# Performance work log

Measured on AMD Instinct MI355X. Metric: run time of the kernel, lower is better.

The kernel has to match this reference:

```python
import jax, jax.numpy as jnp
import numpy as np

N_NODES = 1_000_000
N_UPD = 200_000
D_MEM = 172
D_MSG = 172


def setup_inputs() -> dict:
    key = jax.random.key(0)
    ks = jax.random.split(key, 8)
    memory = jax.random.normal(ks[0], (N_NODES, D_MEM), dtype=jnp.float32)
    last_update = jnp.zeros((N_NODES,), dtype=jnp.float32)
    # unique node ids (no duplicates, as guaranteed by the caller in the original code)
    unique_node_ids = jax.random.permutation(ks[1], N_NODES)[:N_UPD].astype(jnp.int64)
    unique_messages = jax.random.normal(ks[2], (N_UPD, D_MSG), dtype=jnp.float32)
    timestamps = jax.random.uniform(ks[3], (N_UPD,), dtype=jnp.float32) * 1e6
    s_ih = 1.0 / np.sqrt(D_MEM)
    weight_ih = jax.random.uniform(ks[4], (3 * D_MEM, D_MSG), jnp.float32, -s_ih, s_ih)
    weight_hh = jax.random.uniform(ks[5], (3 * D_MEM, D_MEM), jnp.float32, -s_ih, s_ih)
    bias_ih = jax.random.uniform(ks[6], (3 * D_MEM,), jnp.float32, -s_ih, s_ih)
    bias_hh = jax.random.uniform(ks[7], (3 * D_MEM,), jnp.float32, -s_ih, s_ih)
    return {
        "memory": memory,
        "last_update": last_update,
        "unique_node_ids": unique_node_ids,
        "unique_messages": unique_messages,
        "timestamps": timestamps,
        "weight_ih": weight_ih,
        "weight_hh": weight_hh,
        "bias_ih": bias_ih,
        "bias_hh": bias_hh,
    }


def _gru_cell(x, h, weight_ih, weight_hh, bias_ih, bias_hh):
    # PyTorch GRUCell, gate order: reset, update, new
    gi = x @ weight_ih.T + bias_ih          # [M, 3H]
    gh = h @ weight_hh.T + bias_hh          # [M, 3H]
    i_r, i_z, i_n = jnp.split(gi, 3, axis=-1)
    h_r, h_z, h_n = jnp.split(gh, 3, axis=-1)
    r = jax.nn.sigmoid(i_r + h_r)
    z = jax.nn.sigmoid(i_z + h_z)
    n = jnp.tanh(i_n + r * h_n)
    return n + z * (h - n)                  # (1-z)*n + z*h


def reference(memory, last_update, unique_node_ids, unique_messages, timestamps,
              weight_ih, weight_hh, bias_ih, bias_hh):
    # gather rows of the node memory for the updated nodes
    h = memory[unique_node_ids]                                   # [M, D]
    h_new = _gru_cell(unique_messages, h, weight_ih, weight_hh, bias_ih, bias_hh)
    # scatter updated rows back (ids are unique)
    updated_memory = memory.at[unique_node_ids].set(h_new)        # [N, D]
    updated_last_update = last_update.at[unique_node_ids].set(timestamps)
    # original module returns memory with the singleton middle dim restored
    return updated_memory[:, None, :], updated_last_update
```

## Files before the change

### kernel.cpp

```cpp
#include <hip/hip_runtime.h>

typedef __attribute__((ext_vector_type(8))) short short8;
typedef __attribute__((ext_vector_type(4))) float f32x4;

#define N_NODES 1000000
#define N_UPD   200000
#define D       172
#define BM      64
#define LDA     360
#define KSTEPS  11
#define NTILES  48
#define KSLICE  (NTILES*512)
#define GRU_BLOCKS (N_UPD / BM)
#define NM4 43000000
#define BPACK_USHORTS (KSTEPS*KSLICE)
#define BIAS_OFF  (BPACK_USHORTS*2)
#define MASK_OFF  (BIAS_OFF + 688*4)
#define WS_NEED   (MASK_OFF + N_NODES)

__device__ __forceinline__ unsigned short f2bf(float f) {
  union { float f; unsigned u; } v; v.f = f;
  unsigned r = v.u + 0x7FFFu + ((v.u >> 16) & 1u);
  return (unsigned short)(r >> 16);
}
__device__ __forceinline__ float bf2f(unsigned short h) {
  union { unsigned u; float f; } v; v.u = ((unsigned)h) << 16;
  return v.f;
}
__device__ __forceinline__ ushort4 f2bf4(float4 v) {
  return make_ushort4(f2bf(v.x), f2bf(v.y), f2bf(v.z), f2bf(v.w));
}

__device__ __forceinline__ void gld16(const unsigned short* g, unsigned short* l) {
  __builtin_amdgcn_global_load_lds(
      (const __attribute__((address_space(1))) unsigned int*)g,
      (__attribute__((address_space(3))) unsigned int*)l, 16, 0, 0);
}

__global__ void prep_kernel(const float* __restrict__ wih, const float* __restrict__ whh,
                            const float* __restrict__ bih, const float* __restrict__ bhh,
                            unsigned short* __restrict__ Bpack, float* __restrict__ bias4,
                            uint4* __restrict__ mask16) {
  int gid = blockIdx.x * 256 + threadIdx.x;
  if (gid < 688) {
    int which = gid / 172, j = gid % 172;
    float v;
    if (which == 0)      v = bih[j]       + bhh[j];
    else if (which == 1) v = bih[172 + j] + bhh[172 + j];
    else if (which == 2) v = bih[344 + j];
    else                 v = bhh[344 + j];
    bias4[gid] = v;
  }
  if (gid < N_NODES / 16) mask16[gid] = make_uint4(0, 0, 0, 0);
  if (gid >= BPACK_USHORTS) return;
  int e  = gid & 7;
  int l  = (gid >> 3) & 63;
  int nt = (gid >> 9) % NTILES;
  int ks = gid / KSLICE;
  int k  = ks * 32 + ((l >> 4) << 3) + e;
  int c  = l & 15;
  int w  = nt / 12, tl = nt % 12;
  int gate = tl / 3, ti = tl % 3;
  int j = w * 48 + ti * 16 + c;
  float v = 0.f;
  if (j < D) {
    if (gate == 0) {
      if (k < D)        v = wih[j * D + k];
      else if (k < 2*D) v = whh[j * D + (k - D)];
    } else if (gate == 1) {
      if (k < D)        v = wih[(D + j) * D + k];
      else if (k < 2*D) v = whh[(D + j) * D + (k - D)];
    } else if (gate == 2) {
      if (k < D)        v = wih[(2*D + j) * D + k];
    } else {
      if (k >= D && k < 2*D) v = whh[(2*D + j) * D + (k - D)];
    }
  }
  Bpack[gid] = f2bf(v);
}

__global__ void mask_set_kernel(const int* __restrict__ ids, unsigned char* __restrict__ mask) {
  int i = blockIdx.x * 256 + threadIdx.x;
  if (i < N_UPD) mask[ids[i]] = 1;
}

__global__ void copy_kernel(const float4* __restrict__ mem4, const float4* __restrict__ lu4,
                            float4* __restrict__ out4, float4* __restrict__ outlu4) {
  const long NL4 = N_NODES / 4;
  long stride = (long)gridDim.x * blockDim.x;
  for (long i = (long)blockIdx.x * blockDim.x + threadIdx.x; i < NM4 + NL4; i += stride) {
    if (i < NM4) out4[i] = mem4[i];
    else         outlu4[i - NM4] = lu4[i - NM4];
  }
}

__global__ __launch_bounds__(256)
void copy_masked_kernel(const float4* __restrict__ mem4, const float* __restrict__ lu,
                        const unsigned char* __restrict__ mask,
                        float4* __restrict__ out4, float* __restrict__ outlu) {
  const unsigned stride = gridDim.x * 256;
  for (unsigned i = blockIdx.x * 256 + threadIdx.x; i < NM4; i += stride) {
    unsigned row = i / 43u;
    if (!mask[row]) out4[i] = mem4[i];
  }
  for (unsigned j = blockIdx.x * 256 + threadIdx.x; j < N_NODES; j += stride) {
    if (!mask[j]) outlu[j] = lu[j];
  }
}

__global__ __launch_bounds__(512, 2)
void gru64_kernel(const float* __restrict__ memory, const float* __restrict__ msgs,
                  const int* __restrict__ ids, const float* __restrict__ ts,
                  const unsigned short* __restrict__ Bpack, const float* __restrict__ bias4,
                  float* __restrict__ out_mem, float* __restrict__ out_lu) {
  __shared__ unsigned short At[BM * LDA];
  __shared__ unsigned short Bl[2][KSLICE];
  const int tid  = threadIdx.x;
  const int m0   = blockIdx.x * BM;
  const int wave = tid >> 6, lane = tid & 63;
  const int g = lane >> 4, c = lane & 15;
  const int wm = wave >> 2, wc = wave & 3;

  {
    const unsigned short* src = Bpack;
    #pragma unroll
    for (int i = 0; i < 6; ++i) {
      int off = (wave * 6 + i) * 512 + lane * 8;
      gld16(src + off, &Bl[0][0] + off);
    }
  }

  const float4* x4 = (const float4*)msgs + (size_t)m0 * 43;
  float4 xv[6], hv[6];
  #pragma unroll
  for (int i = 0; i < 6; ++i) {
    int s = tid + i * 512;
    if (i < 5 || s < 2752) xv[i] = x4[s];
  }
  #pragma unroll
  for (int i = 0; i < 6; ++i) {
    int s = tid + i * 512;
    if (i < 5 || s < 2752) {
      int row = s / 43, seg = s - row * 43;
      int nid = ids[m0 + row];
      hv[i] = ((const float4*)(memory + (size_t)nid * D))[seg];
    }
  }
  #pragma unroll
  for (int i = 0; i < 6; ++i) {
    int s = tid + i * 512;
    if (i < 5 || s < 2752) {
      int row = s / 43, seg = s - row * 43;
      *(ushort4*)&At[row * LDA + seg * 4]       = f2bf4(xv[i]);
      *(ushort4*)&At[row * LDA + 172 + seg * 4] = f2bf4(hv[i]);
    }
  }
  if (tid < BM) {
    *(uint4*)&At[tid * LDA + 344] = make_uint4(0, 0, 0, 0);
    int nid = ids[m0 + tid];
    out_lu[nid] = ts[m0 + tid];
  }
  __syncthreads();

  f32x4 C0_0={0,0,0,0}, C0_1={0,0,0,0}, C0_2={0,0,0,0}, C0_3={0,0,0,0};
  f32x4 C0_4={0,0,0,0}, C0_5={0,0,0,0}, C0_6={0,0,0,0}, C0_7={0,0,0,0};
  f32x4 C0_8={0,0,0,0}, C0_9={0,0,0,0}, C0_10={0,0,0,0}, C0_11={0,0,0,0};
  f32x4 C1_0={0,0,0,0}, C1_1={0,0,0,0}, C1_2={0,0,0,0}, C1_3={0,0,0,0};
  f32x4 C1_4={0,0,0,0}, C1_5={0,0,0,0}, C1_6={0,0,0,0}, C1_7={0,0,0,0};
  f32x4 C1_8={0,0,0,0}, C1_9={0,0,0,0}, C1_10={0,0,0,0}, C1_11={0,0,0,0};

  const int ar0 = (wm * 32 + c) * LDA;
  const int ar1 = (wm * 32 + 16 + c) * LDA;

#define MMSTEP(NT) { short8 b = bb[(NT)*64]; \
    C0_##NT = __builtin_amdgcn_mfma_f32_16x16x32_bf16(a0, b, C0_##NT, 0, 0, 0); \
    C1_##NT = __builtin_amdgcn_mfma_f32_16x16x32_bf16(a1, b, C1_##NT, 0, 0, 0); }
  int cur = 0;
  #pragma unroll 1
  for (int ks = 0; ks < KSTEPS; ++ks) {
    if (ks + 1 < KSTEPS) {
      const unsigned short* src = Bpack + (size_t)(ks + 1) * KSLICE;
      unsigned short* dst = &Bl[cur ^ 1][0];
      #pragma unroll
      for (int i = 0; i < 6; ++i) {
        int off = (wave * 6 + i) * 512 + lane * 8;
        gld16(src + off, dst + off);
      }
    }
    short8 a0 = *(const short8*)&At[ar0 + ks * 32 + g * 8];
    short8 a1 = *(const short8*)&At[ar1 + ks * 32 + g * 8];
    const short8* bb = (const short8*)&Bl[cur][wc * 12 * 512 + lane * 8];
    MMSTEP(0)  MMSTEP(1)  MMSTEP(2)  MMSTEP(3)
    MMSTEP(4)  MMSTEP(5)  MMSTEP(6)  MMSTEP(7)
    MMSTEP(8)  MMSTEP(9)  MMSTEP(10) MMSTEP(11)
    __syncthreads();
    cur ^= 1;
  }
#undef MMSTEP

#define DO_TI(TI, CR, CZ, CI, CH) { int j = wc * 48 + (TI) * 16 + c; if (j < D) { \
      float rp = CR[r] + bias4[j];        float zp = CZ[r] + bias4[172 + j];      \
      float ip = CI[r] + bias4[344 + j];  float hp = CH[r] + bias4[516 + j];      \
      float ho = bf2f(hrow[j]);                                                   \
      float rr = 1.f / (1.f + __expf(-rp));                                       \
      float zz = 1.f / (1.f + __expf(-zp));                                       \
      float e2 = __expf(2.f * (ip + rr * hp));                                    \
      float nn = 1.f - 2.f / (e2 + 1.f);                                          \
      orow[j] = nn + zz * (ho - nn); } }
  #pragma unroll
  for (int r = 0; r < 4; ++r) {
    {
      const int row_local = wm * 32 + g * 4 + r;
      float* orow = out_mem + (size_t)ids[m0 + row_local] * D;
      const unsigned short* hrow = &At[row_local * LDA + 172];
      DO_TI(0, C0_0, C0_3, C0_6, C0_9)
      DO_TI(1, C0_1, C0_4, C0_7, C0_10)
      DO_TI(2, C0_2, C0_5, C0_8, C0_11)
    }
    {
      const int row_local = wm * 32 + 16 + g * 4 + r;
      float* orow = out_mem + (size_t)ids[m0 + row_local] * D;
      const unsigned short* hrow = &At[row_local * LDA + 172];
      DO_TI(0, C1_0, C1_3, C1_6, C1_9)
      DO_TI(1, C1_1, C1_4, C1_7, C1_10)
      DO_TI(2, C1_2, C1_5, C1_8, C1_11)
    }
  }
#undef DO_TI
}

extern "C" void kernel_launch(void* const* d_in, const int* in_sizes, int n_in,
                              void* d_out, int out_size, void* d_ws, size_t ws_size,
                              hipStream_t stream) {
  const float* memory      = (const float*)d_in[0];
  const float* last_update = (const float*)d_in[1];
  const int*   ids         = (const int*)  d_in[2];
  const float* msgs        = (const float*)d_in[3];
  const float* ts          = (const float*)d_in[4];
  const float* wih         = (const float*)d_in[5];
  const float* whh         = (const float*)d_in[6];
  const float* bih         = (const float*)d_in[7];
  const float* bhh         = (const float*)d_in[8];

  float* out_mem = (float*)d_out;
  float* out_lu  = out_mem + (size_t)N_NODES * D;

  unsigned short* Bpack = (unsigned short*)d_ws;
  float* bias4 = (float*)((char*)d_ws + BIAS_OFF);
  unsigned char* mask = (unsigned char*)d_ws + MASK_OFF;

  prep_kernel<<<BPACK_USHORTS / 256, 256, 0, stream>>>(wih, whh, bih, bhh, Bpack, bias4,
                                                       (uint4*)mask);
  if (ws_size >= WS_NEED) {
    mask_set_kernel<<<(N_UPD + 255) / 256, 256, 0, stream>>>(ids, mask);
    copy_masked_kernel<<<2048, 256, 0, stream>>>((const float4*)memory, last_update, mask,
                                                 (float4*)out_mem, out_lu);
  } else {
    copy_kernel<<<4096, 256, 0, stream>>>((const float4*)memory, (const float4*)last_update,
                                          (float4*)out_mem, (float4*)out_lu);
  }
  gru64_kernel<<<GRU_BLOCKS, 512, 0, stream>>>(memory, msgs, ids, ts, Bpack, bias4,
                                               out_mem, out_lu);
}
```

Before: 589.3 us.

## Fuse masked copy and GRU into one interleaved kernel with larger tiles

Merges the masked memory copy and the GRU kernel into a single launch whose blocks are interleaved between copy work and GRU tiles, so bandwidth-bound copying overlaps with MFMA compute. The GRU tile grows from 64 to 96 rows with 768 threads, and the B-slice double buffer in LDS is replaced by a single buffer that is prefetched through registers and guarded by two barriers per k-step. The aim is to cut the separate copy pass's serialization and raise occupancy, at the cost of extra barriers and tail guards.

```diff
diff --git a/kernel.cpp b/kernel.cpp
--- a/kernel.cpp
+++ b/kernel.cpp
@@ -6,12 +6,17 @@
 #define N_NODES 1000000
 #define N_UPD   200000
 #define D       172
-#define BM      64
+#define BM      96
+#define THREADS 768
 #define LDA     360
 #define KSTEPS  11
 #define NTILES  48
 #define KSLICE  (NTILES*512)
-#define GRU_BLOCKS (N_UPD / BM)
+#define NGRU    2084
+#define NGRU_G  261
+#define NCOPY_G 512
+#define NCOPY_BLOCKS 4096
+#define COPY_THREADS (NCOPY_BLOCKS*THREADS)
 #define NM4 43000000
 #define BPACK_USHORTS (KSTEPS*KSLICE)
 #define BIAS_OFF  (BPACK_USHORTS*2)
@@ -30,7 +35,6 @@
 __device__ __forceinline__ ushort4 f2bf4(float4 v) {
   return make_ushort4(f2bf(v.x), f2bf(v.y), f2bf(v.z), f2bf(v.w));
 }
-
 __device__ __forceinline__ void gld16(const unsigned short* g, unsigned short* l) {
   __builtin_amdgcn_global_load_lds(
       (const __attribute__((address_space(1))) unsigned int*)g,
@@ -94,71 +98,75 @@
   }
 }
 
-__global__ __launch_bounds__(256)
-void copy_masked_kernel(const float4* __restrict__ mem4, const float* __restrict__ lu,
-                        const unsigned char* __restrict__ mask,
-                        float4* __restrict__ out4, float* __restrict__ outlu) {
-  const unsigned stride = gridDim.x * 256;
-  for (unsigned i = blockIdx.x * 256 + threadIdx.x; i < NM4; i += stride) {
-    unsigned row = i / 43u;
-    if (!mask[row]) out4[i] = mem4[i];
-  }
-  for (unsigned j = blockIdx.x * 256 + threadIdx.x; j < N_NODES; j += stride) {
-    if (!mask[j]) outlu[j] = lu[j];
-  }
-}
-
-__global__ __launch_bounds__(512, 2)
-void gru64_kernel(const float* __restrict__ memory, const float* __restrict__ msgs,
-                  const int* __restrict__ ids, const float* __restrict__ ts,
-                  const unsigned short* __restrict__ Bpack, const float* __restrict__ bias4,
-                  float* __restrict__ out_mem, float* __restrict__ out_lu) {
+__global__ __launch_bounds__(THREADS, 3)
+void fused_kernel(const float* __restrict__ memory, const float* __restrict__ last_update,
+                  const float* __restrict__ msgs, const int* __restrict__ ids,
+                  const float* __restrict__ ts, const unsigned short* __restrict__ Bpack,
+                  const float* __restrict__ bias4, const unsigned char* __restrict__ mask,
+                  float* __restrict__ out_mem, float* __restrict__ out_lu, int ncopyg) {
   __shared__ unsigned short At[BM * LDA];
-  __shared__ unsigned short Bl[2][KSLICE];
-  const int tid  = threadIdx.x;
-  const int m0   = blockIdx.x * BM;
+  __shared__ unsigned short Bl[KSLICE];
+  const int tid = threadIdx.x;
+  const int g8 = blockIdx.x >> 3, b7 = blockIdx.x & 7;
+
+  int sub; bool is_copy = false;
+  if (ncopyg) {
+    int r = g8 % 3, q = g8 / 3;
+    if (r == 0) sub = q;
+    else { is_copy = true; sub = q * 2 + (r - 1); if (sub >= NCOPY_G) return; }
+  } else sub = g8;
+
+  if (is_copy) {
+    const int cblk = sub * 8 + b7;
+    const float4* mem4 = (const float4*)memory;
+    float4* out4 = (float4*)out_mem;
+    for (unsigned i = (unsigned)cblk * THREADS + tid; i < NM4; i += COPY_THREADS) {
+      unsigned row = i / 43u;
+      if (!mask[row]) out4[i] = mem4[i];
+    }
+    for (unsigned j = (unsigned)cblk * THREADS + tid; j < N_NODES; j += COPY_THREADS) {
+      if (!mask[j]) out_lu[j] = last_update[j];
+    }
+    return;
+  }
+
+  const int idx = sub * 8 + b7;
+  const int m0  = idx * BM;
+  if (m0 >= N_UPD) return;
   const int wave = tid >> 6, lane = tid & 63;
   const int g = lane >> 4, c = lane & 15;
   const int wm = wave >> 2, wc = wave & 3;
 
-  {
-    const unsigned short* src = Bpack;
-    #pragma unroll
-    for (int i = 0; i < 6; ++i) {
-      int off = (wave * 6 + i) * 512 + lane * 8;
-      gld16(src + off, &Bl[0][0] + off);
-    }
-  }
-
+  #pragma unroll
+  for (int i = 0; i < 4; ++i) {
+    int off = (wave * 4 + i) * 512 + lane * 8;
+    gld16(Bpack + off, &Bl[0] + off);
+  }
+
+  const int vlim = min(BM * 43, (N_UPD - m0) * 43);
   const float4* x4 = (const float4*)msgs + (size_t)m0 * 43;
   float4 xv[6], hv[6];
   #pragma unroll
   for (int i = 0; i < 6; ++i) {
-    int s = tid + i * 512;
-    if (i < 5 || s < 2752) xv[i] = x4[s];
+    int s = tid + i * THREADS; int sc = min(s, vlim - 1);
+    xv[i] = x4[sc];
   }
   #pragma unroll
   for (int i = 0; i < 6; ++i) {
-    int s = tid + i * 512;
-    if (i < 5 || s < 2752) {
-      int row = s / 43, seg = s - row * 43;
-      int nid = ids[m0 + row];
-      hv[i] = ((const float4*)(memory + (size_t)nid * D))[seg];
-    }
+    int s = tid + i * THREADS; int sc = min(s, vlim - 1);
+    int row = sc / 43, seg = sc - row * 43;
+    hv[i] = ((const float4*)(memory + (size_t)ids[m0 + row] * D))[seg];
   }
   #pragma unroll
   for (int i = 0; i < 6; ++i) {
-    int s = tid + i * 512;
-    if (i < 5 || s < 2752) {
-      int row = s / 43, seg = s - row * 43;
-      *(ushort4*)&At[row * LDA + seg * 4]       = f2bf4(xv[i]);
-      *(ushort4*)&At[row * LDA + 172 + seg * 4] = f2bf4(hv[i]);
-    }
+    int s = tid + i * THREADS; int sc = min(s, vlim - 1);
+    int row = sc / 43, seg = sc - row * 43;
+    *(ushort4*)&At[row * LDA + seg * 4]       = f2bf4(xv[i]);
+    *(ushort4*)&At[row * LDA + 172 + seg * 4] = f2bf4(hv[i]);
   }
   if (tid < BM) {
     *(uint4*)&At[tid * LDA + 344] = make_uint4(0, 0, 0, 0);
-    int nid = ids[m0 + tid];
-    out_lu[nid] = ts[m0 + tid];
+    if (m0 + tid < N_UPD) out_lu[ids[m0 + tid]] = ts[m0 + tid];
   }
   __syncthreads();
 
@@ -170,31 +178,32 @@
   f32x4 C1_8={0,0,0,0}, C1_9={0,0,0,0}, C1_10={0,0,0,0}, C1_11={0,0,0,0};
 
   const int ar0 = (wm * 32 + c) * LDA;
-  const int ar1 = (wm * 32 + 16 + c) * LDA;
+  const int ar1 = ar0 + 16 * LDA;
+  const int boff = (wave * 4) * 64 + lane;
 
 #define MMSTEP(NT) { short8 b = bb[(NT)*64]; \
     C0_##NT = __builtin_amdgcn_mfma_f32_16x16x32_bf16(a0, b, C0_##NT, 0, 0, 0); \
     C1_##NT = __builtin_amdgcn_mfma_f32_16x16x32_bf16(a1, b, C1_##NT, 0, 0, 0); }
-  int cur = 0;
   #pragma unroll 1
   for (int ks = 0; ks < KSTEPS; ++ks) {
-    if (ks + 1 < KSTEPS) {
-      const unsigned short* src = Bpack + (size_t)(ks + 1) * KSLICE;
-      unsigned short* dst = &Bl[cur ^ 1][0];
-      #pragma unroll
-      for (int i = 0; i < 6; ++i) {
-        int off = (wave * 6 + i) * 512 + lane * 8;
-        gld16(src + off, dst + off);
-      }
+    float4 s0, s1, s2, s3;
+    const bool pf = (ks + 1 < KSTEPS);
+    if (pf) {
+      const float4* bsrc = (const float4*)(Bpack + (size_t)(ks + 1) * KSLICE) + boff;
+      s0 = bsrc[0]; s1 = bsrc[64]; s2 = bsrc[128]; s3 = bsrc[192];
     }
     short8 a0 = *(const short8*)&At[ar0 + ks * 32 + g * 8];
     short8 a1 = *(const short8*)&At[ar1 + ks * 32 + g * 8];
-    const short8* bb = (const short8*)&Bl[cur][wc * 12 * 512 + lane * 8];
+    const short8* bb = (const short8*)&Bl[wc * 6144 + lane * 8];
     MMSTEP(0)  MMSTEP(1)  MMSTEP(2)  MMSTEP(3)
     MMSTEP(4)  MMSTEP(5)  MMSTEP(6)  MMSTEP(7)
     MMSTEP(8)  MMSTEP(9)  MMSTEP(10) MMSTEP(11)
-    __syncthreads();
-    cur ^= 1;
+    if (pf) {
+      __syncthreads();
+      float4* bdst = (float4*)Bl + boff;
+      bdst[0] = s0; bdst[64] = s1; bdst[128] = s2; bdst[192] = s3;
+      __syncthreads();
+    }
   }
 #undef MMSTEP
 
@@ -211,19 +220,23 @@
   for (int r = 0; r < 4; ++r) {
     {
       const int row_local = wm * 32 + g * 4 + r;
-      float* orow = out_mem + (size_t)ids[m0 + row_local] * D;
-      const unsigned short* hrow = &At[row_local * LDA + 172];
-      DO_TI(0, C0_0, C0_3, C0_6, C0_9)
-      DO_TI(1, C0_1, C0_4, C0_7, C0_10)
-      DO_TI(2, C0_2, C0_5, C0_8, C0_11)
+      if (m0 + row_local < N_UPD) {
+        float* orow = out_mem + (size_t)ids[m0 + row_local] * D;
+        const unsigned short* hrow = &At[row_local * LDA + 172];
+        DO_TI(0, C0_0, C0_3, C0_6, C0_9)
+        DO_TI(1, C0_1, C0_4, C0_7, C0_10)
+        DO_TI(2, C0_2, C0_5, C0_8, C0_11)
+      }
     }
     {
       const int row_local = wm * 32 + 16 + g * 4 + r;
-      float* orow = out_mem + (size_t)ids[m0 + row_local] * D;
-      const unsigned short* hrow = &At[row_local * LDA + 172];
-      DO_TI(0, C1_0, C1_3, C1_6, C1_9)
-      DO_TI(1, C1_1, C1_4, C1_7, C1_10)
-      DO_TI(2, C1_2, C1_5, C1_8, C1_11)
+      if (m0 + row_local < N_UPD) {
+        float* orow = out_mem + (size_t)ids[m0 + row_local] * D;
+        const unsigned short* hrow = &At[row_local * LDA + 172];
+        DO_TI(0, C1_0, C1_3, C1_6, C1_9)
+        DO_TI(1, C1_1, C1_4, C1_7, C1_10)
+        DO_TI(2, C1_2, C1_5, C1_8, C1_11)
+      }
     }
   }
 #undef DO_TI
@@ -253,12 +266,12 @@
                                                        (uint4*)mask);
   if (ws_size >= WS_NEED) {
     mask_set_kernel<<<(N_UPD + 255) / 256, 256, 0, stream>>>(ids, mask);
-    copy_masked_kernel<<<2048, 256, 0, stream>>>((const float4*)memory, last_update, mask,
-                                                 (float4*)out_mem, out_lu);
+    fused_kernel<<<NGRU_G * 3 * 8, THREADS, 0, stream>>>(
+        memory, last_update, msgs, ids, ts, Bpack, bias4, mask, out_mem, out_lu, NCOPY_G);
   } else {
     copy_kernel<<<4096, 256, 0, stream>>>((const float4*)memory, (const float4*)last_update,
                                           (float4*)out_mem, (float4*)out_lu);
-  }
-  gru64_kernel<<<GRU_BLOCKS, 512, 0, stream>>>(memory, msgs, ids, ts, Bpack, bias4,
-                                               out_mem, out_lu);
-}
+    fused_kernel<<<NGRU_G * 8, THREADS, 0, stream>>>(
+        memory, last_update, msgs, ids, ts, Bpack, bias4, mask, out_mem, out_lu, 0);
+  }
+}
```

Result: no change. 577.9 us (-1.9%).

## Drop LDS weight staging; stream B fragments from global per output tile

Applied to the files above, without the earlier changes.

Removes the double-buffered LDS copy of the packed weights and the per-k-step barriers. Each wave now loops over its three 16-column output tiles, loading B fragments straight from global memory (relying on L2/cache) and keeping only 8 accumulators live. It also skips the empty fourth tile for the last wave group. With less LDS and fewer registers in use, launch bounds are raised to 4 blocks per CU to improve latency hiding on the gather-heavy kernel. The cost is repeated global reads of the weights per block instead of a shared LDS copy.

```diff
diff --git a/kernel.cpp b/kernel.cpp
--- a/kernel.cpp
+++ b/kernel.cpp
@@ -29,12 +29,6 @@
 }
 __device__ __forceinline__ ushort4 f2bf4(float4 v) {
   return make_ushort4(f2bf(v.x), f2bf(v.y), f2bf(v.z), f2bf(v.w));
-}
-
-__device__ __forceinline__ void gld16(const unsigned short* g, unsigned short* l) {
-  __builtin_amdgcn_global_load_lds(
-      (const __attribute__((address_space(1))) unsigned int*)g,
-      (__attribute__((address_space(3))) unsigned int*)l, 16, 0, 0);
 }
 
 __global__ void prep_kernel(const float* __restrict__ wih, const float* __restrict__ whh,
@@ -108,27 +102,17 @@
   }
 }
 
-__global__ __launch_bounds__(512, 2)
+__global__ __launch_bounds__(512, 4)
 void gru64_kernel(const float* __restrict__ memory, const float* __restrict__ msgs,
                   const int* __restrict__ ids, const float* __restrict__ ts,
                   const unsigned short* __restrict__ Bpack, const float* __restrict__ bias4,
                   float* __restrict__ out_mem, float* __restrict__ out_lu) {
   __shared__ unsigned short At[BM * LDA];
-  __shared__ unsigned short Bl[2][KSLICE];
   const int tid  = threadIdx.x;
   const int m0   = blockIdx.x * BM;
   const int wave = tid >> 6, lane = tid & 63;
   const int g = lane >> 4, c = lane & 15;
   const int wm = wave >> 2, wc = wave & 3;
-
-  {
-    const unsigned short* src = Bpack;
-    #pragma unroll
-    for (int i = 0; i < 6; ++i) {
-      int off = (wave * 6 + i) * 512 + lane * 8;
-      gld16(src + off, &Bl[0][0] + off);
-    }
-  }
 
   const float4* x4 = (const float4*)msgs + (size_t)m0 * 43;
   float4 xv[6], hv[6];
@@ -142,8 +126,7 @@
     int s = tid + i * 512;
     if (i < 5 || s < 2752) {
       int row = s / 43, seg = s - row * 43;
-      int nid = ids[m0 + row];
-      hv[i] = ((const float4*)(memory + (size_t)nid * D))[seg];
+      hv[i] = ((const float4*)(memory + (size_t)ids[m0 + row] * D))[seg];
     }
   }
   #pragma unroll
@@ -157,76 +140,74 @@
   }
   if (tid < BM) {
     *(uint4*)&At[tid * LDA + 344] = make_uint4(0, 0, 0, 0);
-    int nid = ids[m0 + tid];
-    out_lu[nid] = ts[m0 + tid];
+    out_lu[ids[m0 + tid]] = ts[m0 + tid];
   }
   __syncthreads();
 
-  f32x4 C0_0={0,0,0,0}, C0_1={0,0,0,0}, C0_2={0,0,0,0}, C0_3={0,0,0,0};
-  f32x4 C0_4={0,0,0,0}, C0_5={0,0,0,0}, C0_6={0,0,0,0}, C0_7={0,0,0,0};
-  f32x4 C0_8={0,0,0,0}, C0_9={0,0,0,0}, C0_10={0,0,0,0}, C0_11={0,0,0,0};
-  f32x4 C1_0={0,0,0,0}, C1_1={0,0,0,0}, C1_2={0,0,0,0}, C1_3={0,0,0,0};
-  f32x4 C1_4={0,0,0,0}, C1_5={0,0,0,0}, C1_6={0,0,0,0}, C1_7={0,0,0,0};
-  f32x4 C1_8={0,0,0,0}, C1_9={0,0,0,0}, C1_10={0,0,0,0}, C1_11={0,0,0,0};
-
   const int ar0 = (wm * 32 + c) * LDA;
-  const int ar1 = (wm * 32 + 16 + c) * LDA;
-
-#define MMSTEP(NT) { short8 b = bb[(NT)*64]; \
-    C0_##NT = __builtin_amdgcn_mfma_f32_16x16x32_bf16(a0, b, C0_##NT, 0, 0, 0); \
-    C1_##NT = __builtin_amdgcn_mfma_f32_16x16x32_bf16(a1, b, C1_##NT, 0, 0, 0); }
-  int cur = 0;
+  const int ar1 = ar0 + 16 * LDA;
+  const short8* Bp = (const short8*)Bpack;
+
   #pragma unroll 1
-  for (int ks = 0; ks < KSTEPS; ++ks) {
-    if (ks + 1 < KSTEPS) {
-      const unsigned short* src = Bpack + (size_t)(ks + 1) * KSLICE;
-      unsigned short* dst = &Bl[cur ^ 1][0];
+  for (int ti = 0; ti < 3; ++ti) {
+    if (wc == 3 && ti == 2) continue;
+    const short8* bp = Bp + (size_t)((wc * 12 + ti) * 64 + lane);
+
+    f32x4 Cr0={0,0,0,0}, Cr1={0,0,0,0};
+    f32x4 Cz0={0,0,0,0}, Cz1={0,0,0,0};
+    f32x4 Ci0={0,0,0,0}, Ci1={0,0,0,0};
+    f32x4 Ch0={0,0,0,0}, Ch1={0,0,0,0};
+
+    #pragma unroll 2
+    for (int ks = 0; ks < KSTEPS; ++ks) {
+      const short8* bk = bp + ks * 3072;
+      short8 br = bk[0];
+      short8 bz = bk[192];
+      short8 bi = bk[384];
+      short8 bh = bk[576];
+      short8 a0 = *(const short8*)&At[ar0 + ks * 32 + g * 8];
+      short8 a1 = *(const short8*)&At[ar1 + ks * 32 + g * 8];
+      Cr0 = __builtin_amdgcn_mfma_f32_16x16x32_bf16(a0, br, Cr0, 0, 0, 0);
+      Cr1 = __builtin_amdgcn_mfma_f32_16x16x32_bf16(a1, br, Cr1, 0, 0, 0);
+      Cz0 = __builtin_amdgcn_mfma_f32_16x16x32_bf16(a0, bz, Cz0, 0, 0, 0);
+      Cz1 = __builtin_amdgcn_mfma_f32_16x16x32_bf16(a1, bz, Cz1, 0, 0, 0);
+      Ci0 = __builtin_amdgcn_mfma_f32_16x16x32_bf16(a0, bi, Ci0, 0, 0, 0);
+      Ci1 = __builtin_amdgcn_mfma_f32_16x16x32_bf16(a1, bi, Ci1, 0, 0, 0);
+      Ch0 = __builtin_amdgcn_mfma_f32_16x16x32_bf16(a0, bh, Ch0, 0, 0, 0);
+      Ch1 = __builtin_amdgcn_mfma_f32_16x16x32_bf16(a1, bh, Ch1, 0, 0, 0);
+    }
+
+    const int j = wc * 48 + ti * 16 + c;
+    if (j < D) {
+      const float b_r = bias4[j];
+      const float b_z = bias4[172 + j];
+      const float b_i = bias4[344 + j];
+      const float b_h = bias4[516 + j];
       #pragma unroll
-      for (int i = 0; i < 6; ++i) {
-        int off = (wave * 6 + i) * 512 + lane * 8;
-        gld16(src + off, dst + off);
+      for (int r = 0; r < 4; ++r) {
+        {
+          const int row_local = wm * 32 + g * 4 + r;
+          float* orow = out_mem + (size_t)ids[m0 + row_local] * D;
+          float ho = bf2f(At[row_local * LDA + 172 + j]);
+          float rr = 1.f / (1.f + __expf(-(Cr0[r] + b_r)));
+          float zz = 1.f / (1.f + __expf(-(Cz0[r] + b_z)));
+          float e2 = __expf(2.f * (Ci0[r] + b_i + rr * (Ch0[r] + b_h)));
+          float nn = 1.f - 2.f / (e2 + 1.f);
+          orow[j] = nn + zz * (ho - nn);
+        }
+        {
+          const int row_local = wm * 32 + 16 + g * 4 + r;
+          float* orow = out_mem + (size_t)ids[m0 + row_local] * D;
+          float ho = bf2f(At[row_local * LDA + 172 + j]);
+          float rr = 1.f / (1.f + __expf(-(Cr1[r] + b_r)));
+          float zz = 1.f / (1.f + __expf(-(Cz1[r] + b_z)));
+          float e2 = __expf(2.f * (Ci1[r] + b_i + rr * (Ch1[r] + b_h)));
+          float nn = 1.f - 2.f / (e2 + 1.f);
+          orow[j] = nn + zz * (ho - nn);
+        }
       }
     }
-    short8 a0 = *(const short8*)&At[ar0 + ks * 32 + g * 8];
-    short8 a1 = *(const short8*)&At[ar1 + ks * 32 + g * 8];
-    const short8* bb = (const short8*)&Bl[cur][wc * 12 * 512 + lane * 8];
-    MMSTEP(0)  MMSTEP(1)  MMSTEP(2)  MMSTEP(3)
-    MMSTEP(4)  MMSTEP(5)  MMSTEP(6)  MMSTEP(7)
-    MMSTEP(8)  MMSTEP(9)  MMSTEP(10) MMSTEP(11)
-    __syncthreads();
-    cur ^= 1;
-  }
-#undef MMSTEP
-
-#define DO_TI(TI, CR, CZ, CI, CH) { int j = wc * 48 + (TI) * 16 + c; if (j < D) { \
-      float rp = CR[r] + bias4[j];        float zp = CZ[r] + bias4[172 + j];      \
-      float ip = CI[r] + bias4[344 + j];  float hp = CH[r] + bias4[516 + j];      \
-      float ho = bf2f(hrow[j]);                                                   \
-      float rr = 1.f / (1.f + __expf(-rp));                                       \
-      float zz = 1.f / (1.f + __expf(-zp));                                       \
-      float e2 = __expf(2.f * (ip + rr * hp));                                    \
-      float nn = 1.f - 2.f / (e2 + 1.f);                                          \
-      orow[j] = nn + zz * (ho - nn); } }
-  #pragma unroll
-  for (int r = 0; r < 4; ++r) {
-    {
-      const int row_local = wm * 32 + g * 4 + r;
-      float* orow = out_mem + (size_t)ids[m0 + row_local] * D;
-      const unsigned short* hrow = &At[row_local * LDA + 172];
-      DO_TI(0, C0_0, C0_3, C0_6, C0_9)
-      DO_TI(1, C0_1, C0_4, C0_7, C0_10)
-      DO_TI(2, C0_2, C0_5, C0_8, C0_11)
-    }
-    {
-      const int row_local = wm * 32 + 16 + g * 4 + r;
-      float* orow = out_mem + (size_t)ids[m0 + row_local] * D;
-      const unsigned short* hrow = &At[row_local * LDA + 172];
-      DO_TI(0, C1_0, C1_3, C1_6, C1_9)
-      DO_TI(1, C1_1, C1_4, C1_7, C1_10)
-      DO_TI(2, C1_2, C1_5, C1_8, C1_11)
-    }
-  }
-#undef DO_TI
+  }
 }
 
 extern "C" void kernel_launch(void* const* d_in, const int* in_sizes, int n_in,
```

New measurement: 492.7 us. -16.4%, faster.
